# Kernel tuning notes

Hardware: AMD Instinct MI355X
Metric: run time of the kernel (lower is better)

The kernel has to match this reference:

```python
import jax, jax.numpy as jnp
import numpy as np


def setup_inputs() -> dict:
    key = jax.random.key(0)
    k1, k2 = jax.random.split(key)
    B, G, P = 64, 4999, 50
    raw_gene_expr = jax.random.normal(k1, (B, G), dtype=jnp.float32)
    # binary pathway membership matrix, mimics torch.randint(0, 2, (P, G)).float()
    pathway_gene_matrix = (jax.random.uniform(k2, (P, G)) < 0.5).astype(jnp.float32)
    return {"raw_gene_expr": raw_gene_expr, "pathway_gene_matrix": pathway_gene_matrix}


def reference(raw_gene_expr, pathway_gene_matrix):
    """Vectorized ssGSEA enrichment (compute_pathway_activations0).

    raw_gene_expr:        [B, G] float
    pathway_gene_matrix:  [P, G] binary float
    returns:              [B, P] signed max-deviation enrichment scores
    """
    B, G = raw_gene_expr.shape
    P = pathway_gene_matrix.shape[0]

    # Sort genes per sample in descending expression order
    order = jnp.argsort(-raw_gene_expr, axis=1)                      # [B, G]
    sorted_expr = jnp.take_along_axis(raw_gene_expr, order, axis=1)  # [B, G]

    # hit[b, p, i] = 1 if gene at sorted position i belongs to pathway p
    hit = (pathway_gene_matrix[:, order] > 0)                        # [P, B, G]
    hit = jnp.transpose(hit, (1, 0, 2)).astype(raw_gene_expr.dtype)  # [B, P, G]

    size = jnp.sum(pathway_gene_matrix > 0, axis=1).astype(raw_gene_expr.dtype)  # [P]

    # Weighted hit increments: |expr|^0.25 over hits, normalized per (sample, pathway)
    w = (jnp.abs(sorted_expr) ** 0.25)[:, None, :] * hit             # [B, P, G]
    s = jnp.sum(w, axis=-1, keepdims=True)
    w = jnp.where(s > 0, w / jnp.where(s > 0, s, 1.0), w)

    cum_hit = jnp.cumsum(w, axis=-1)                                 # [B, P, G]
    denom = jnp.maximum(G - size, 1.0)[None, :, None]                # guard size==G
    cum_miss = jnp.cumsum((1.0 - hit) / denom, axis=-1)              # [B, P, G]

    running = cum_hit - cum_miss                                     # [B, P, G]
    pos = jnp.argmax(jnp.abs(running), axis=-1)                      # [B, P]
    # signed max deviation == running value at the argmax of |running|
    es = jnp.take_along_axis(running, pos[..., None], axis=-1)[..., 0]  # [B, P]
    es = jnp.where(size[None, :] > 0, es, 0.0)
    return es
```

## Files before the change

kernel.cpp:

```cpp
#include <hip/hip_runtime.h>
#include <math.h>

typedef unsigned long long ull;

constexpr int Bc = 64;
constexpr int Gc = 4999;
constexpr int Pc = 50;

constexpr int RUN   = 1024;
constexpr int NRUN  = 5;
constexpr int NPAD  = NRUN * RUN;
constexpr int LPW4  = 21;
constexpr int PADG  = 256 * LPW4;
constexpr int QSPAN = 64 * LPW4;
constexpr ull PADKEY = 0xFFFFFFFFFFFFFFFFull;

__device__ __forceinline__ ull shfl_xor64(ull v, int lm) {
    int lo = __shfl_xor((int)(unsigned)(v & 0xFFFFFFFFull), lm, 64);
    int hi = __shfl_xor((int)(unsigned)(v >> 32), lm, 64);
    return ((ull)(unsigned)hi << 32) | (unsigned)lo;
}

__global__ __launch_bounds__(256) void chunk_sort(
    const float* __restrict__ expr, const float* __restrict__ pathway,
    ull* __restrict__ runs, ull* __restrict__ pbits, int P, int G)
{
    __shared__ ull key[RUN];
    const int r = blockIdx.x, b = blockIdx.y, tid = threadIdx.x;
    const int base = tid * 4;
    const float* row = expr + (size_t)b * G;

    ull v[4];
#pragma unroll
    for (int o = 0; o < 4; ++o) {
        int i = r * RUN + base + o;
        if (i < G) {
            unsigned u = __float_as_uint(row[i]);
            unsigned m = (u >> 31) ? ~u : (u | 0x80000000u);
            v[o] = ((ull)(~m) << 32) | (unsigned)i;
        } else {
            v[o] = PADKEY;
        }
    }

    for (int kk = 2; kk <= RUN; kk <<= 1) {
        const int j0 = kk >> 1;
        if (j0 >= 256) {
#pragma unroll
            for (int o = 0; o < 4; ++o) key[base + o] = v[o];
            __syncthreads();
            for (int j = j0; j >= 256; j >>= 1) {
#pragma unroll
                for (int t = tid; t < RUN / 2; t += 256) {
                    int i  = ((t & ~(j - 1)) << 1) | (t & (j - 1));
                    int ix = i | j;
                    ull a = key[i], c = key[ix];
                    bool up = ((i & kk) == 0);
                    if ((a > c) == up) { key[i] = c; key[ix] = a; }
                }
                __syncthreads();
            }
#pragma unroll
            for (int o = 0; o < 4; ++o) v[o] = key[base + o];
        }
        int jstart = (j0 > 128) ? 128 : j0;
        for (int j = jstart; j >= 4; j >>= 1) {
            int lm = j >> 2;
            bool takeMin = (((tid & lm) == 0) == ((base & kk) == 0));
#pragma unroll
            for (int o = 0; o < 4; ++o) {
                ull c = shfl_xor64(v[o], lm);
                ull mn = (v[o] < c) ? v[o] : c;
                ull mx = (v[o] < c) ? c : v[o];
                v[o] = takeMin ? mn : mx;
            }
        }
#pragma unroll
        for (int j = 2; j >= 1; j >>= 1) {
            if (j < kk) {
#pragma unroll
                for (int o = 0; o < 4; ++o) {
                    if ((o & j) == 0) {
                        bool up = (((base + o) & kk) == 0);
                        ull a = v[o], c = v[o | j];
                        if ((a > c) == up) { v[o] = c; v[o | j] = a; }
                    }
                }
            }
        }
    }

    ull* dst = runs + ((size_t)b * NRUN + r) * RUN;
#pragma unroll
    for (int o = 0; o < 4; ++o) dst[base + o] = v[o];

    if (r == 0) {
        int g = b * 256 + tid;
        if (g < G) {
            ull m = 0;
#pragma unroll
            for (int p = 0; p < Pc; ++p)
                if (pathway[(size_t)p * G + g] > 0.0f) m |= (1ull << p);
            pbits[g] = m;
        }
    }
}

__global__ __launch_bounds__(1024) void rank_scatter(
    const ull* __restrict__ runs, const ull* __restrict__ pbits,
    ulonglong2* __restrict__ wp, int G)
{
    __shared__ ull runsLDS[NPAD];
    const int rg = blockIdx.x, b = blockIdx.y, tid = threadIdx.x;

    const ull* rowruns = runs + (size_t)b * NPAD;
    for (int i = tid; i < NPAD; i += 1024) runsLDS[i] = rowruns[i];
    __syncthreads();

    const int e = rg * 1024 + tid;
    const ull keyv = runsLDS[e];
    if (keyv == PADKEY) return;

    const int idx = (int)(unsigned)(keyv & 0xFFFFFFFFu);
    const ull pb = pbits[idx];

    const int run = e >> 10;
    int rank = e & 1023;
#pragma unroll
    for (int rr = 0; rr < NRUN; ++rr) {
        if (rr == run) continue;
        const ull* arr = &runsLDS[rr * RUN];
        int pos = 0;
#pragma unroll
        for (int s = RUN; s >= 1; s >>= 1) {
            int np = pos + s;
            if (np <= RUN && arr[np - 1] < keyv) pos = np;
        }
        rank += pos;
    }

    unsigned m = ~((unsigned)(keyv >> 32));
    unsigned absbits = ((m >> 31) ? m : ~m) & 0x7FFFFFFFu;
    float av = __uint_as_float(absbits);
    ulonglong2 t;
    t.x = pb;
    t.y = (ull)__float_as_uint(sqrtf(sqrtf(av)));
    wp[(size_t)b * G + rank] = t;
}

__global__ __launch_bounds__(1024) void es_kernel(
    const ulonglong2* __restrict__ wp, float* __restrict__ out,
    int B, int P, int G)
{
    __shared__ float    swq[PADG];
    __shared__ unsigned sm32[PADG];
    __shared__ double   cSW[4][4][4];
    __shared__ int      cSH[4][4][4];
    __shared__ double   cBV[4][4][4];
    __shared__ double   cBR[4][4][4];

    const int pg = blockIdx.x;
    const int b  = blockIdx.y;
    const int tid = threadIdx.x;
    const int pbeg = pg * 13;
    const int pend = (pbeg + 13 < P) ? (pbeg + 13) : P;

    for (int i = tid; i < PADG; i += 1024) {
        if (i < G) {
            ulonglong2 t = wp[(size_t)b * G + i];
            swq[i]  = __uint_as_float((unsigned)t.y);
            sm32[i] = (unsigned)(t.x >> pbeg);
        } else {
            swq[i]  = 0.0f;
            sm32[i] = 0xFFFFFFFFu;
        }
    }
    __syncthreads();

    const int lane = tid & 63;
    const int w  = tid >> 6;
    const int qg = w >> 2;
    const int h  = w & 3;
    const int sh4 = qg * 4;

    const int lg = h * 64 + lane;
    const int start = lg * LPW4;
    int npads = start + LPW4 - G;
    npads = (npads < 0) ? 0 : ((npads > LPW4) ? LPW4 : npads);

    double sw[4] = {0.0, 0.0, 0.0, 0.0};
    int shl[4] = {0, 0, 0, 0};
#pragma unroll
    for (int k = 0; k < LPW4; ++k) {
        int s = start + k;
        unsigned b4 = sm32[s] >> sh4;
        double wv = (double)swq[s];
#pragma unroll
        for (int q = 0; q < 4; ++q) {
            if ((b4 >> q) & 1u) { sw[q] += wv; shl[q]++; }
        }
    }
#pragma unroll
    for (int q = 0; q < 4; ++q) {
        double s_ = sw[q]; int c_ = shl[q] - npads;
#pragma unroll
        for (int off = 1; off < 64; off <<= 1) {
            s_ += __shfl_xor(s_, off, 64);
            c_ += __shfl_xor(c_, off, 64);
        }
        if (lane == 0) { cSW[qg][h][q] = s_; cSH[qg][h][q] = c_; }
    }
    __syncthreads();

    int Qc[4];
#pragma unroll
    for (int hh = 0; hh < 4; ++hh) {
        int c = G - hh * QSPAN;
        Qc[hh] = (c < 0) ? 0 : ((c > QSPAN) ? QSPAN : c);
    }

    double negE[4], normq[4], runn[4];
    int shtot[4];
#pragma unroll
    for (int q = 0; q < 4; ++q) {
        double st = 0.0; int ct = 0;
#pragma unroll
        for (int hh = 0; hh < 4; ++hh) { st += cSW[qg][hh][q]; ct += cSH[qg][hh][q]; }
        shtot[q] = ct;
        double d = 1.0 / fmax((double)(G - ct), 1.0);
        double e = (st > 0.0) ? d * st : d;
        negE[q]  = -e;
        normq[q] = (st > 0.0) ? 1.0 / st : 1.0;
        double offq = 0.0;
        for (int hh = 0; hh < h; ++hh)
            offq += cSW[qg][hh][q] - (double)(Qc[hh] - cSH[qg][hh][q]) * e;
        double csum = sw[q] - (double)(LPW4 - shl[q]) * e;
        double x = csum;
#pragma unroll
        for (int off = 1; off < 64; off <<= 1) {
            double vv = __shfl_up(x, off, 64);
            if (lane >= off) x += vv;
        }
        runn[q] = x - csum + offq;
    }

    double bestv[4] = {-1.0, -1.0, -1.0, -1.0};
    double bestr[4] = {0.0, 0.0, 0.0, 0.0};
    int besti[4] = {0x7FFFFFFF, 0x7FFFFFFF, 0x7FFFFFFF, 0x7FFFFFFF};
#pragma unroll
    for (int k = 0; k < LPW4; ++k) {
        int s = start + k;
        unsigned b4 = sm32[s] >> sh4;
        double wv = (double)swq[s];
#pragma unroll
        for (int q = 0; q < 4; ++q) {
            runn[q] += ((b4 >> q) & 1u) ? wv : negE[q];
            double a = fabs(runn[q]);
            if (a > bestv[q]) { bestv[q] = a; bestr[q] = runn[q]; besti[q] = s; }
        }
    }
#pragma unroll
    for (int q = 0; q < 4; ++q) {
#pragma unroll
        for (int off = 1; off < 64; off <<= 1) {
            double ov  = __shfl_xor(bestv[q], off, 64);
            double orr = __shfl_xor(bestr[q], off, 64);
            int    oi  = __shfl_xor(besti[q], off, 64);
            if (ov > bestv[q] || (ov == bestv[q] && oi < besti[q])) {
                bestv[q] = ov; bestr[q] = orr; besti[q] = oi;
            }
        }
        if (lane == 0) { cBV[qg][h][q] = bestv[q]; cBR[qg][h][q] = bestr[q]; }
    }
    __syncthreads();

    if (h == 0 && lane == 0) {
#pragma unroll
        for (int q = 0; q < 4; ++q) {
            double bv = cBV[qg][0][q];
            double br = cBR[qg][0][q];
#pragma unroll
            for (int hh = 1; hh < 4; ++hh) {
                double v_ = cBV[qg][hh][q];
                if (v_ > bv) { bv = v_; br = cBR[qg][hh][q]; }
            }
            int p = pbeg + sh4 + q;
            if (p < pend)
                out[(size_t)b * P + p] =
                    (shtot[q] > 0) ? (float)(br * normq[q]) : 0.0f;
        }
    }
}

extern "C" void kernel_launch(void* const* d_in, const int* in_sizes, int n_in,
                              void* d_out, int out_size, void* d_ws, size_t ws_size,
                              hipStream_t stream) {
    const float* expr    = (const float*)d_in[0];
    const float* pathway = (const float*)d_in[1];
    float* out = (float*)d_out;

    char* ws = (char*)d_ws;
    ull*        pbits = (ull*)ws;
    ull*        runs  = (ull*)(ws + 40960);
    ulonglong2* wp    = (ulonglong2*)(ws + 2662400);

    chunk_sort<<<dim3(NRUN, Bc), dim3(256), 0, stream>>>(
        expr, pathway, runs, pbits, Pc, Gc);
    rank_scatter<<<dim3(NRUN, Bc), dim3(1024), 0, stream>>>(runs, pbits, wp, Gc);
    es_kernel<<<dim3(4, Bc), dim3(1024), 0, stream>>>(
        wp, out, Bc, Pc, Gc);
}
```

Before: 103.9 us.

## Sort eight keys per thread and split rank scatter into smaller blocks

The per-run bitonic sort now uses 128 threads with eight keys each. This removes the LDS-based merge stage at j=256, so only j=512 goes through shared memory, and it adds float4 input loads and 128-bit output stores. The rank_scatter kernel now uses 256-thread blocks on a 20x64 grid instead of 1024-thread blocks, with vectorized LDS fills. The aim is fewer barriers and better occupancy and scheduling. The cost is more register pressure per thread and each block redundantly loading the full 40KB row into LDS; the float4 loads also assume unaligned global access is tolerated.

New measurement: 115.6 us. 1.11x slower.

```diff
diff --git a/kernel.cpp b/kernel.cpp
--- a/kernel.cpp
+++ b/kernel.cpp
@@ -10,6 +10,8 @@
 constexpr int RUN   = 1024;
 constexpr int NRUN  = 5;
 constexpr int NPAD  = NRUN * RUN;
+constexpr int TC    = 128;
+constexpr int EC    = 8;
 constexpr int LPW4  = 21;
 constexpr int PADG  = 256 * LPW4;
 constexpr int QSPAN = 64 * LPW4;
@@ -21,54 +23,69 @@
     return ((ull)(unsigned)hi << 32) | (unsigned)lo;
 }
 
-__global__ __launch_bounds__(256) void chunk_sort(
+__global__ __launch_bounds__(TC) void chunk_sort(
     const float* __restrict__ expr, const float* __restrict__ pathway,
     ull* __restrict__ runs, ull* __restrict__ pbits, int P, int G)
 {
     __shared__ ull key[RUN];
     const int r = blockIdx.x, b = blockIdx.y, tid = threadIdx.x;
-    const int base = tid * 4;
+    const int lane = tid & 63;
+    const int base = tid * EC;
     const float* row = expr + (size_t)b * G;
-
-    ull v[4];
-#pragma unroll
-    for (int o = 0; o < 4; ++o) {
-        int i = r * RUN + base + o;
-        if (i < G) {
-            unsigned u = __float_as_uint(row[i]);
-            unsigned m = (u >> 31) ? ~u : (u | 0x80000000u);
-            v[o] = ((ull)(~m) << 32) | (unsigned)i;
-        } else {
-            v[o] = PADKEY;
+    const int gbase = r * RUN + base;
+
+    ull v[EC];
+    if (gbase + EC <= G) {
+        const float4* row4 = (const float4*)(row + r * RUN);
+#pragma unroll
+        for (int f = 0; f < 2; ++f) {
+            float4 x = row4[tid * 2 + f];
+            float xs[4] = {x.x, x.y, x.z, x.w};
+#pragma unroll
+            for (int c = 0; c < 4; ++c) {
+                int o = f * 4 + c;
+                unsigned u = __float_as_uint(xs[c]);
+                unsigned m = (u >> 31) ? ~u : (u | 0x80000000u);
+                v[o] = ((ull)(~m) << 32) | (unsigned)(gbase + o);
+            }
+        }
+    } else {
+#pragma unroll
+        for (int o = 0; o < EC; ++o) {
+            int i = gbase + o;
+            if (i < G) {
+                unsigned u = __float_as_uint(row[i]);
+                unsigned m = (u >> 31) ? ~u : (u | 0x80000000u);
+                v[o] = ((ull)(~m) << 32) | (unsigned)i;
+            } else {
+                v[o] = PADKEY;
+            }
         }
     }
 
     for (int kk = 2; kk <= RUN; kk <<= 1) {
         const int j0 = kk >> 1;
-        if (j0 >= 256) {
-#pragma unroll
-            for (int o = 0; o < 4; ++o) key[base + o] = v[o];
+        if (j0 >= 512) {
+#pragma unroll
+            for (int o = 0; o < EC; ++o) key[base + o] = v[o];
             __syncthreads();
-            for (int j = j0; j >= 256; j >>= 1) {
-#pragma unroll
-                for (int t = tid; t < RUN / 2; t += 256) {
-                    int i  = ((t & ~(j - 1)) << 1) | (t & (j - 1));
-                    int ix = i | j;
-                    ull a = key[i], c = key[ix];
-                    bool up = ((i & kk) == 0);
-                    if ((a > c) == up) { key[i] = c; key[ix] = a; }
-                }
-                __syncthreads();
-            }
-#pragma unroll
-            for (int o = 0; o < 4; ++o) v[o] = key[base + o];
-        }
-        int jstart = (j0 > 128) ? 128 : j0;
-        for (int j = jstart; j >= 4; j >>= 1) {
-            int lm = j >> 2;
-            bool takeMin = (((tid & lm) == 0) == ((base & kk) == 0));
-#pragma unroll
-            for (int o = 0; o < 4; ++o) {
+            for (int t = tid; t < RUN / 2; t += TC) {
+                int i  = t;
+                int ix = t | 512;
+                ull a = key[i], c = key[ix];
+                bool up = ((i & kk) == 0);
+                if ((a > c) == up) { key[i] = c; key[ix] = a; }
+            }
+            __syncthreads();
+#pragma unroll
+            for (int o = 0; o < EC; ++o) v[o] = key[base + o];
+        }
+        int jstart = (j0 > 256) ? 256 : j0;
+        for (int j = jstart; j >= EC; j >>= 1) {
+            int lm = j >> 3;
+            bool takeMin = (((lane & lm) == 0) == ((base & kk) == 0));
+#pragma unroll
+            for (int o = 0; o < EC; ++o) {
                 ull c = shfl_xor64(v[o], lm);
                 ull mn = (v[o] < c) ? v[o] : c;
                 ull mx = (v[o] < c) ? c : v[o];
@@ -76,10 +93,10 @@
             }
         }
 #pragma unroll
-        for (int j = 2; j >= 1; j >>= 1) {
+        for (int j = 4; j >= 1; j >>= 1) {
             if (j < kk) {
 #pragma unroll
-                for (int o = 0; o < 4; ++o) {
+                for (int o = 0; o < EC; ++o) {
                     if ((o & j) == 0) {
                         bool up = (((base + o) & kk) == 0);
                         ull a = v[o], c = v[o | j];
@@ -90,12 +107,15 @@
         }
     }
 
-    ull* dst = runs + ((size_t)b * NRUN + r) * RUN;
-#pragma unroll
-    for (int o = 0; o < 4; ++o) dst[base + o] = v[o];
+    ulonglong2* dst2 = (ulonglong2*)(runs + ((size_t)b * NRUN + r) * RUN + base);
+#pragma unroll
+    for (int o = 0; o < EC; o += 2) {
+        ulonglong2 t; t.x = v[o]; t.y = v[o + 1];
+        dst2[o / 2] = t;
+    }
 
     if (r == 0) {
-        int g = b * 256 + tid;
+        int g = b * TC + tid;
         if (g < G) {
             ull m = 0;
 #pragma unroll
@@ -106,18 +126,19 @@
     }
 }
 
-__global__ __launch_bounds__(1024) void rank_scatter(
+__global__ __launch_bounds__(256) void rank_scatter(
     const ull* __restrict__ runs, const ull* __restrict__ pbits,
     ulonglong2* __restrict__ wp, int G)
 {
     __shared__ ull runsLDS[NPAD];
     const int rg = blockIdx.x, b = blockIdx.y, tid = threadIdx.x;
 
-    const ull* rowruns = runs + (size_t)b * NPAD;
-    for (int i = tid; i < NPAD; i += 1024) runsLDS[i] = rowruns[i];
+    const ulonglong2* r2 = (const ulonglong2*)(runs + (size_t)b * NPAD);
+    ulonglong2* l2 = (ulonglong2*)runsLDS;
+    for (int i = tid; i < NPAD / 2; i += 256) l2[i] = r2[i];
     __syncthreads();
 
-    const int e = rg * 1024 + tid;
+    const int e = rg * 256 + tid;
     const ull keyv = runsLDS[e];
     if (keyv == PADKEY) return;
 
@@ -304,9 +325,9 @@
     ull*        runs  = (ull*)(ws + 40960);
     ulonglong2* wp    = (ulonglong2*)(ws + 2662400);
 
-    chunk_sort<<<dim3(NRUN, Bc), dim3(256), 0, stream>>>(
+    chunk_sort<<<dim3(NRUN, Bc), dim3(TC), 0, stream>>>(
         expr, pathway, runs, pbits, Pc, Gc);
-    rank_scatter<<<dim3(NRUN, Bc), dim3(1024), 0, stream>>>(runs, pbits, wp, Gc);
+    rank_scatter<<<dim3(20, Bc), dim3(256), 0, stream>>>(runs, pbits, wp, Gc);
     es_kernel<<<dim3(4, Bc), dim3(1024), 0, stream>>>(
         wp, out, Bc, Pc, Gc);
 }
```
